# Kernel optimization log

Measured on AMD Instinct MI355X. Metric: run time of the kernel, lower is better.

Reference implementation:

```python
import jax, jax.numpy as jnp
import numpy as np

C, H, W = 16, 128, 128   # in_features, dim0, dim1
FD, OUT, POOL = 3, 64, 2  # filter_dim, out_features, pooling
B = 32


def setup_inputs() -> dict:
    key = jax.random.key(0)
    k1, k2, k3 = jax.random.split(key, 3)
    x = jax.random.normal(k1, (B, C, H, W), dtype=jnp.float32)
    # linear_layer: weight (in*fd^2, out) scaled by 1/sqrt(in*fd^2), bias (out,)
    weight = jax.random.normal(k2, (C * FD * FD, OUT), dtype=jnp.float32) / jnp.sqrt(
        jnp.float32(C * FD * FD))
    bias = jax.random.normal(k3, (OUT,), dtype=jnp.float32)
    return {"x": x, "weight": weight, "bias": bias}


def reference(x, weight, bias):
    # The one-hot isometry tensordot + reshape is exactly im2col with patch
    # vector ordering c*FD^2 + n*FD + m, so the whole convolution() equals a
    # VALID conv with kernel[o, c, n, m] = weight[c*FD^2 + n*FD + m, o].
    kernel = weight.reshape(C, FD, FD, OUT).transpose(3, 0, 1, 2)  # OIHW
    y = jax.lax.conv_general_dilated(
        x, kernel, window_strides=(1, 1), padding='VALID',
        dimension_numbers=('NCHW', 'OIHW', 'NCHW'))  # (B, OUT, n_conv, m_conv)
    y = jax.nn.relu(y + bias[None, :, None, None])
    b, o, hc, wc = y.shape  # hc = H-FD+1 = 126
    # block max-pool POOLxPOOL (crop to multiple of POOL, as in the original)
    hp, wp = hc // POOL, wc // POOL
    y = y[:, :, :hp * POOL, :wp * POOL].reshape(b, o, hp, POOL, wp, POOL)
    y = jnp.max(y, axis=(3, 5))  # (B, OUT, hp, wp)
    return y.reshape(b, o, -1)  # (B, OUT, hp*wp)
```

## Files before the change

kernel.cpp:

```cpp
#include <hip/hip_runtime.h>


typedef _Float16 f16x8 __attribute__((ext_vector_type(8)));
typedef float f32x16 __attribute__((ext_vector_type(16)));

#define MFMA16(A, B, C) __builtin_amdgcn_mfma_f32_32x32x16_f16(A, B, C, 0, 0, 0)

__global__ void convert_w(const float* __restrict__ weight, char* __restrict__ ws) {
  int tau = blockIdx.x * 256 + threadIdx.x;
  if (tau >= 1152) return;
  int t = tau >> 7, r = tau & 127, o = r >> 1, hf = r & 1;
  _Float16 h[8];
#pragma unroll
  for (int j = 0; j < 8; ++j)
    h[j] = (_Float16)weight[((hf * 8 + j) * 9 + t) * 64 + o];
  int off = (t * 2 + (o >> 5)) * 1024 + (hf * 32 + (o & 31)) * 16;
  *(f16x8*)(ws + off) = *(f16x8*)h;
}

__device__ __forceinline__ void compute_step(const char* lds, const f16x8 W[9][2],
                                             f32x16 acc[2][2], int i2, int xbase) {
#pragma unroll
  for (int q = 0; q < 16; ++q) {
    acc[0][0][q] = 0.f; acc[0][1][q] = 0.f;
    acc[1][0][q] = 0.f; acc[1][1][q] = 0.f;
  }
  __builtin_amdgcn_s_setprio(1);
#pragma unroll
  for (int t = 0; t < 9; ++t) {
    const int n = t / 3, m = t - 3 * n;
    const int a0 = (i2 + n) * 4096 + xbase + m * 16;
    const int a1 = a0 + 4096;
    f16x8 X0 = *(const f16x8*)(lds + a0);
    f16x8 X1 = *(const f16x8*)(lds + a1);
    acc[0][0] = MFMA16(W[t][0], X0, acc[0][0]);
    acc[1][0] = MFMA16(W[t][1], X0, acc[1][0]);
    acc[0][1] = MFMA16(W[t][0], X1, acc[0][1]);
    acc[1][1] = MFMA16(W[t][1], X1, acc[1][1]);
  }
  __builtin_amdgcn_s_setprio(0);
}

__device__ __forceinline__ void epilogue(const f32x16 acc[2][2],
                                         const float* __restrict__ bias,
                                         float* __restrict__ out, int b, int pr,
                                         int wv, int lane) {
  const int c31 = lane & 31;
  const int half = lane >> 5;
  const int pw = wv * 16 + (c31 >> 1);
  const bool doit = ((c31 & 1) == 0) && (pw < 63);
  const int obase = ((b * 64) * 63 + pr) * 63 + pw;
#pragma unroll
  for (int ot = 0; ot < 2; ++ot) {
#pragma unroll
    for (int q = 0; q < 16; ++q) {
      const int o0 = ot * 32 + (q & 3) + 8 * (q >> 2);
      float v = fmaxf(acc[ot][0][q], acc[ot][1][q]);
      v = fmaxf(v, __shfl_xor(v, 1, 64));
      float bv = half ? bias[o0 + 4] : bias[o0];
      v = fmaxf(v + bv, 0.0f);
      if (doit) out[obase + (o0 + 4 * half) * 3969] = v;
    }
  }
}

__global__ __launch_bounds__(256, 3)
void convpool_main(const float* __restrict__ x, const char* __restrict__ ws,
                   const float* __restrict__ bias, float* __restrict__ out) {
  __shared__ __align__(16) char lds[24640];
  const int tid = threadIdx.x;
  const int s = blockIdx.x;
  const int b = blockIdx.y;
  const int rb = 4 * s;
  const bool two = (s < 31);
  const int nr = two ? 6 : 4;
  const int lane = tid & 63;
  const int wv = tid >> 6;
  const int colS = tid >> 1;
  const int hfS = tid & 1;
  const float* xb = x + (b * 16 + hfS * 8) * 16384 + colS;

  float pv[6][8];
#pragma unroll
  for (int r = 0; r < 6; ++r)
    if (r < nr) {
#pragma unroll
      for (int j = 0; j < 8; ++j) pv[r][j] = xb[j * 16384 + (rb + r) * 128];
    }

  f16x8 W[9][2];
#pragma unroll
  for (int t = 0; t < 9; ++t)
#pragma unroll
    for (int ot = 0; ot < 2; ++ot)
      W[t][ot] = *(const f16x8*)(ws + (t * 2 + ot) * 1024 + lane * 16);

#pragma unroll
  for (int r = 0; r < 6; ++r)
    if (r < nr) {
      _Float16 h[8];
#pragma unroll
      for (int j = 0; j < 8; ++j) h[j] = (_Float16)pv[r][j];
      *(f16x8*)(lds + r * 4096 + hfS * 2048 + colS * 16) = *(f16x8*)h;
    }
  __syncthreads();

  const int xbase = (lane >> 5) * 2048 + (wv * 32 + (lane & 31)) * 16;
  f32x16 acc[2][2];

  compute_step(lds, W, acc, 0, xbase);
  epilogue(acc, bias, out, b, 2 * s, wv, lane);
  if (two) {
    compute_step(lds, W, acc, 2, xbase);
    epilogue(acc, bias, out, b, 2 * s + 1, wv, lane);
  }
}

extern "C" void kernel_launch(void* const* d_in, const int* in_sizes, int n_in,
                              void* d_out, int out_size, void* d_ws, size_t ws_size,
                              hipStream_t stream) {
  const float* x = (const float*)d_in[0];
  const float* wgt = (const float*)d_in[1];
  const float* bias = (const float*)d_in[2];
  float* out = (float*)d_out;
  char* ws = (char*)d_ws;
  convert_w<<<dim3(5), 256, 0, stream>>>(wgt, ws);
  convpool_main<<<dim3(32, 32), 256, 0, stream>>>(x, ws, bias, out);
}
```

Measured before the change: 45.13 us.

## Split work per block to one pooled row and one output-channel half

Each block now computes a single pooled output row for half of the output channels, so the grid grows from 32x32 to 126x32 blocks. Weights for that half are staged through LDS instead of being held in registers, which cuts register use and allows the launch bound to rise to 4 blocks per CU. In exchange, every block reloads its 4 input rows, so global reads of x rise roughly fourfold, and the input conversion is repeated across the channel halves.

```diff
diff --git a/kernel.cpp b/kernel.cpp
--- a/kernel.cpp
+++ b/kernel.cpp
@@ -18,101 +18,82 @@
   *(f16x8*)(ws + off) = *(f16x8*)h;
 }
 
-__device__ __forceinline__ void compute_step(const char* lds, const f16x8 W[9][2],
-                                             f32x16 acc[2][2], int i2, int xbase) {
+__global__ __launch_bounds__(256, 4)
+void convpool_main(const float* __restrict__ x, const char* __restrict__ ws,
+                   const float* __restrict__ bias, float* __restrict__ out) {
+  __shared__ __align__(16) char lds[25664];
+  const int tid = threadIdx.x;
+  const int bx = blockIdx.x;
+  const int pr = bx >> 1;
+  const int oh = bx & 1;
+  const int b = blockIdx.y;
+  const int lane = tid & 63;
+  const int wv = tid >> 6;
+  const int colS = tid >> 1;
+  const int hfS = tid & 1;
+  const float* xb = x + (b * 16 + hfS * 8) * 16384 + colS;
+
+  float pv[4][8];
 #pragma unroll
-  for (int q = 0; q < 16; ++q) {
-    acc[0][0][q] = 0.f; acc[0][1][q] = 0.f;
-    acc[1][0][q] = 0.f; acc[1][1][q] = 0.f;
+  for (int r = 0; r < 4; ++r)
+#pragma unroll
+    for (int j = 0; j < 8; ++j)
+      pv[r][j] = xb[j * 16384 + (2 * pr + r) * 128];
+
+  float4 wc[3];
+#pragma unroll
+  for (int k = 0; k < 3; ++k) {
+    int idx = tid + 256 * k;
+    if (idx < 576) {
+      int tap = idx >> 6, off = idx & 63;
+      wc[k] = *(const float4*)(ws + (tap * 2 + oh) * 1024 + off * 16);
+    }
   }
-  __builtin_amdgcn_s_setprio(1);
+
+#pragma unroll
+  for (int k = 0; k < 3; ++k) {
+    int idx = tid + 256 * k;
+    if (idx < 576) {
+      int tap = idx >> 6, off = idx & 63;
+      *(float4*)(lds + tap * 1024 + off * 16) = wc[k];
+    }
+  }
+#pragma unroll
+  for (int r = 0; r < 4; ++r) {
+    _Float16 h[8];
+#pragma unroll
+    for (int j = 0; j < 8; ++j) h[j] = (_Float16)pv[r][j];
+    *(f16x8*)(lds + 9216 + r * 4096 + hfS * 2048 + colS * 16) = *(f16x8*)h;
+  }
+  __syncthreads();
+
+  const int xbase = 9216 + (lane >> 5) * 2048 + (wv * 32 + (lane & 31)) * 16;
+  f32x16 a0, a1;
+#pragma unroll
+  for (int q = 0; q < 16; ++q) { a0[q] = 0.f; a1[q] = 0.f; }
 #pragma unroll
   for (int t = 0; t < 9; ++t) {
     const int n = t / 3, m = t - 3 * n;
-    const int a0 = (i2 + n) * 4096 + xbase + m * 16;
-    const int a1 = a0 + 4096;
-    f16x8 X0 = *(const f16x8*)(lds + a0);
-    f16x8 X1 = *(const f16x8*)(lds + a1);
-    acc[0][0] = MFMA16(W[t][0], X0, acc[0][0]);
-    acc[1][0] = MFMA16(W[t][1], X0, acc[1][0]);
-    acc[0][1] = MFMA16(W[t][0], X1, acc[0][1]);
-    acc[1][1] = MFMA16(W[t][1], X1, acc[1][1]);
+    f16x8 Wt = *(const f16x8*)(lds + t * 1024 + lane * 16);
+    f16x8 X0 = *(const f16x8*)(lds + n * 4096 + xbase + m * 16);
+    f16x8 X1 = *(const f16x8*)(lds + (n + 1) * 4096 + xbase + m * 16);
+    a0 = MFMA16(Wt, X0, a0);
+    a1 = MFMA16(Wt, X1, a1);
   }
-  __builtin_amdgcn_s_setprio(0);
-}
 
-__device__ __forceinline__ void epilogue(const f32x16 acc[2][2],
-                                         const float* __restrict__ bias,
-                                         float* __restrict__ out, int b, int pr,
-                                         int wv, int lane) {
   const int c31 = lane & 31;
   const int half = lane >> 5;
   const int pw = wv * 16 + (c31 >> 1);
   const bool doit = ((c31 & 1) == 0) && (pw < 63);
   const int obase = ((b * 64) * 63 + pr) * 63 + pw;
 #pragma unroll
-  for (int ot = 0; ot < 2; ++ot) {
-#pragma unroll
-    for (int q = 0; q < 16; ++q) {
-      const int o0 = ot * 32 + (q & 3) + 8 * (q >> 2);
-      float v = fmaxf(acc[ot][0][q], acc[ot][1][q]);
-      v = fmaxf(v, __shfl_xor(v, 1, 64));
-      float bv = half ? bias[o0 + 4] : bias[o0];
-      v = fmaxf(v + bv, 0.0f);
-      if (doit) out[obase + (o0 + 4 * half) * 3969] = v;
-    }
-  }
-}
-
-__global__ __launch_bounds__(256, 3)
-void convpool_main(const float* __restrict__ x, const char* __restrict__ ws,
-                   const float* __restrict__ bias, float* __restrict__ out) {
-  __shared__ __align__(16) char lds[24640];
-  const int tid = threadIdx.x;
-  const int s = blockIdx.x;
-  const int b = blockIdx.y;
-  const int rb = 4 * s;
-  const bool two = (s < 31);
-  const int nr = two ? 6 : 4;
-  const int lane = tid & 63;
-  const int wv = tid >> 6;
-  const int colS = tid >> 1;
-  const int hfS = tid & 1;
-  const float* xb = x + (b * 16 + hfS * 8) * 16384 + colS;
-
-  float pv[6][8];
-#pragma unroll
-  for (int r = 0; r < 6; ++r)
-    if (r < nr) {
-#pragma unroll
-      for (int j = 0; j < 8; ++j) pv[r][j] = xb[j * 16384 + (rb + r) * 128];
-    }
-
-  f16x8 W[9][2];
-#pragma unroll
-  for (int t = 0; t < 9; ++t)
-#pragma unroll
-    for (int ot = 0; ot < 2; ++ot)
-      W[t][ot] = *(const f16x8*)(ws + (t * 2 + ot) * 1024 + lane * 16);
-
-#pragma unroll
-  for (int r = 0; r < 6; ++r)
-    if (r < nr) {
-      _Float16 h[8];
-#pragma unroll
-      for (int j = 0; j < 8; ++j) h[j] = (_Float16)pv[r][j];
-      *(f16x8*)(lds + r * 4096 + hfS * 2048 + colS * 16) = *(f16x8*)h;
-    }
-  __syncthreads();
-
-  const int xbase = (lane >> 5) * 2048 + (wv * 32 + (lane & 31)) * 16;
-  f32x16 acc[2][2];
-
-  compute_step(lds, W, acc, 0, xbase);
-  epilogue(acc, bias, out, b, 2 * s, wv, lane);
-  if (two) {
-    compute_step(lds, W, acc, 2, xbase);
-    epilogue(acc, bias, out, b, 2 * s + 1, wv, lane);
+  for (int q = 0; q < 16; ++q) {
+    const int o0 = oh * 32 + (q & 3) + 8 * (q >> 2);
+    float v = fmaxf(a0[q], a1[q]);
+    v = fmaxf(v, __shfl_xor(v, 1, 64));
+    float bv = half ? bias[o0 + 4] : bias[o0];
+    v = fmaxf(v + bv, 0.0f);
+    if (doit) out[obase + (o0 + 4 * half) * 3969] = v;
   }
 }
 
@@ -125,5 +106,5 @@
   float* out = (float*)d_out;
   char* ws = (char*)d_ws;
   convert_w<<<dim3(5), 256, 0, stream>>>(wgt, ws);
-  convpool_main<<<dim3(32, 32), 256, 0, stream>>>(x, ws, bias, out);
+  convpool_main<<<dim3(126, 32), 256, 0, stream>>>(x, ws, bias, out);
 }
```

After: 53.65 us. 18.9% more time.

## Pre-convert input to fp16 workspace and stream tiles via direct global-to-LDS loads

Applied to the files above, without the earlier changes.

Adds a pre-pass kernel that converts the whole fp32 input to a channel-interleaved fp16 layout in workspace, alongside the weight conversion. The main kernel then loads rows straight into LDS with global_load_lds, so it no longer converts in registers. Each block now handles 8 input rows and 4 pooled rows in a loop instead of 2, which cuts halo re-reads. The cost is an extra full pass that reads the fp32 input and writes 16 MB of fp16, plus larger LDS use per block.

```diff
diff --git a/kernel.cpp b/kernel.cpp
--- a/kernel.cpp
+++ b/kernel.cpp
@@ -5,114 +5,106 @@
 typedef float f32x16 __attribute__((ext_vector_type(16)));
 
 #define MFMA16(A, B, C) __builtin_amdgcn_mfma_f32_32x32x16_f16(A, B, C, 0, 0, 0)
+#define XH_BYTES 16777216
 
-__global__ void convert_w(const float* __restrict__ weight, char* __restrict__ ws) {
-  int tau = blockIdx.x * 256 + threadIdx.x;
-  if (tau >= 1152) return;
-  int t = tau >> 7, r = tau & 127, o = r >> 1, hf = r & 1;
-  _Float16 h[8];
+#define GLOAD_LDS16(g, l)                                                    \
+  __builtin_amdgcn_global_load_lds(                                          \
+      (const __attribute__((address_space(1))) void*)(g),                    \
+      (__attribute__((address_space(3))) void*)(l), 16, 0, 0)
+
+__global__ void convert_xw(const float* __restrict__ x,
+                           const float* __restrict__ weight,
+                           char* __restrict__ ws) {
+  const int n = blockIdx.x;
+  if (n < 4096) {
+    const int g = n * 256 + threadIdx.x;
+    const int hf = g & 1, col = (g >> 1) & 127, row = (g >> 8) & 127, b = g >> 15;
+    _Float16 h[8];
 #pragma unroll
-  for (int j = 0; j < 8; ++j)
-    h[j] = (_Float16)weight[((hf * 8 + j) * 9 + t) * 64 + o];
-  int off = (t * 2 + (o >> 5)) * 1024 + (hf * 32 + (o & 31)) * 16;
-  *(f16x8*)(ws + off) = *(f16x8*)h;
-}
-
-__device__ __forceinline__ void compute_step(const char* lds, const f16x8 W[9][2],
-                                             f32x16 acc[2][2], int i2, int xbase) {
+    for (int j = 0; j < 8; ++j)
+      h[j] = (_Float16)x[((b * 16 + hf * 8 + j) * 128 + row) * 128 + col];
+    *(f16x8*)(ws + g * 16) = *(f16x8*)h;
+  } else {
+    const int tau = (n - 4096) * 256 + threadIdx.x;
+    if (tau >= 1152) return;
+    const int t = tau >> 7, r = tau & 127, o = r >> 1, hf = r & 1;
+    _Float16 h[8];
 #pragma unroll
-  for (int q = 0; q < 16; ++q) {
-    acc[0][0][q] = 0.f; acc[0][1][q] = 0.f;
-    acc[1][0][q] = 0.f; acc[1][1][q] = 0.f;
-  }
-  __builtin_amdgcn_s_setprio(1);
-#pragma unroll
-  for (int t = 0; t < 9; ++t) {
-    const int n = t / 3, m = t - 3 * n;
-    const int a0 = (i2 + n) * 4096 + xbase + m * 16;
-    const int a1 = a0 + 4096;
-    f16x8 X0 = *(const f16x8*)(lds + a0);
-    f16x8 X1 = *(const f16x8*)(lds + a1);
-    acc[0][0] = MFMA16(W[t][0], X0, acc[0][0]);
-    acc[1][0] = MFMA16(W[t][1], X0, acc[1][0]);
-    acc[0][1] = MFMA16(W[t][0], X1, acc[0][1]);
-    acc[1][1] = MFMA16(W[t][1], X1, acc[1][1]);
-  }
-  __builtin_amdgcn_s_setprio(0);
-}
-
-__device__ __forceinline__ void epilogue(const f32x16 acc[2][2],
-                                         const float* __restrict__ bias,
-                                         float* __restrict__ out, int b, int pr,
-                                         int wv, int lane) {
-  const int c31 = lane & 31;
-  const int half = lane >> 5;
-  const int pw = wv * 16 + (c31 >> 1);
-  const bool doit = ((c31 & 1) == 0) && (pw < 63);
-  const int obase = ((b * 64) * 63 + pr) * 63 + pw;
-#pragma unroll
-  for (int ot = 0; ot < 2; ++ot) {
-#pragma unroll
-    for (int q = 0; q < 16; ++q) {
-      const int o0 = ot * 32 + (q & 3) + 8 * (q >> 2);
-      float v = fmaxf(acc[ot][0][q], acc[ot][1][q]);
-      v = fmaxf(v, __shfl_xor(v, 1, 64));
-      float bv = half ? bias[o0 + 4] : bias[o0];
-      v = fmaxf(v + bv, 0.0f);
-      if (doit) out[obase + (o0 + 4 * half) * 3969] = v;
-    }
+    for (int j = 0; j < 8; ++j)
+      h[j] = (_Float16)weight[((hf * 8 + j) * 9 + t) * 64 + o];
+    const int off = (t * 2 + (o >> 5)) * 1024 + (hf * 32 + (o & 31)) * 16;
+    *(f16x8*)(ws + XH_BYTES + off) = *(f16x8*)h;
   }
 }
 
 __global__ __launch_bounds__(256, 3)
-void convpool_main(const float* __restrict__ x, const char* __restrict__ ws,
-                   const float* __restrict__ bias, float* __restrict__ out) {
-  __shared__ __align__(16) char lds[24640];
+void convpool_main(const char* __restrict__ ws, const float* __restrict__ bias,
+                   float* __restrict__ out) {
+  __shared__ __align__(16) char lds[41024];
   const int tid = threadIdx.x;
   const int s = blockIdx.x;
   const int b = blockIdx.y;
-  const int rb = 4 * s;
-  const bool two = (s < 31);
-  const int nr = two ? 6 : 4;
+  const int nsteps = (s < 15) ? 4 : 3;
+  const int rb = 8 * s;
   const int lane = tid & 63;
-  const int wv = tid >> 6;
-  const int colS = tid >> 1;
-  const int hfS = tid & 1;
-  const float* xb = x + (b * 16 + hfS * 8) * 16384 + colS;
+  const int ph = tid >> 6;
+  const int half = lane >> 5;
+  const int c31 = lane & 31;
 
-  float pv[6][8];
+  const char* xrow = ws + (size_t)(b * 128 + rb) * 4096 + tid * 16;
 #pragma unroll
-  for (int r = 0; r < 6; ++r)
-    if (r < nr) {
-#pragma unroll
-      for (int j = 0; j < 8; ++j) pv[r][j] = xb[j * 16384 + (rb + r) * 128];
-    }
+  for (int r = 0; r < 10; ++r)
+    if (rb + r < 128)
+      GLOAD_LDS16(xrow + r * 4096, lds + r * 4096 + tid * 16);
 
+  const char* wsW = ws + XH_BYTES;
   f16x8 W[9][2];
 #pragma unroll
   for (int t = 0; t < 9; ++t)
 #pragma unroll
     for (int ot = 0; ot < 2; ++ot)
-      W[t][ot] = *(const f16x8*)(ws + (t * 2 + ot) * 1024 + lane * 16);
+      W[t][ot] = *(const f16x8*)(wsW + (t * 2 + ot) * 1024 + lane * 16);
 
-#pragma unroll
-  for (int r = 0; r < 6; ++r)
-    if (r < nr) {
-      _Float16 h[8];
-#pragma unroll
-      for (int j = 0; j < 8; ++j) h[j] = (_Float16)pv[r][j];
-      *(f16x8*)(lds + r * 4096 + hfS * 2048 + colS * 16) = *(f16x8*)h;
-    }
   __syncthreads();
 
-  const int xbase = (lane >> 5) * 2048 + (wv * 32 + (lane & 31)) * 16;
-  f32x16 acc[2][2];
+  const int xoff = (ph * 32 + c31) * 32 + half * 16;
+  const int pw = ph * 16 + (c31 >> 1);
+  const bool doit = ((c31 & 1) == 0) && (pw < 63);
 
-  compute_step(lds, W, acc, 0, xbase);
-  epilogue(acc, bias, out, b, 2 * s, wv, lane);
-  if (two) {
-    compute_step(lds, W, acc, 2, xbase);
-    epilogue(acc, bias, out, b, 2 * s + 1, wv, lane);
+  for (int i = 0; i < nsteps; ++i) {
+    f32x16 acc[2][2];
+#pragma unroll
+    for (int q = 0; q < 16; ++q) {
+      acc[0][0][q] = 0.f; acc[0][1][q] = 0.f;
+      acc[1][0][q] = 0.f; acc[1][1][q] = 0.f;
+    }
+    __builtin_amdgcn_s_setprio(1);
+#pragma unroll
+    for (int t = 0; t < 9; ++t) {
+      const int n = t / 3, m = t - 3 * n;
+      const int a0 = (2 * i + n) * 4096 + xoff + m * 32;
+      f16x8 X0 = *(const f16x8*)(lds + a0);
+      f16x8 X1 = *(const f16x8*)(lds + a0 + 4096);
+      acc[0][0] = MFMA16(W[t][0], X0, acc[0][0]);
+      acc[1][0] = MFMA16(W[t][1], X0, acc[1][0]);
+      acc[0][1] = MFMA16(W[t][0], X1, acc[0][1]);
+      acc[1][1] = MFMA16(W[t][1], X1, acc[1][1]);
+    }
+    __builtin_amdgcn_s_setprio(0);
+
+    const int p = 4 * s + i;
+    const int obase = ((b * 64) * 63 + p) * 63 + pw;
+#pragma unroll
+    for (int ot = 0; ot < 2; ++ot)
+#pragma unroll
+      for (int q = 0; q < 16; ++q) {
+        const int o0 = ot * 32 + (q & 3) + 8 * (q >> 2);
+        float v = fmaxf(acc[ot][0][q], acc[ot][1][q]);
+        v = fmaxf(v, __shfl_xor(v, 1, 64));
+        const float bv = half ? bias[o0 + 4] : bias[o0];
+        v = fmaxf(v + bv, 0.0f);
+        if (doit) out[obase + (o0 + 4 * half) * 3969] = v;
+      }
   }
 }
 
@@ -124,6 +116,6 @@
   const float* bias = (const float*)d_in[2];
   float* out = (float*)d_out;
   char* ws = (char*)d_ws;
-  convert_w<<<dim3(5), 256, 0, stream>>>(wgt, ws);
-  convpool_main<<<dim3(32, 32), 256, 0, stream>>>(x, ws, bias, out);
+  convert_xw<<<dim3(4101), 256, 0, stream>>>(x, wgt, ws);
+  convpool_main<<<dim3(16, 32), 256, 0, stream>>>(ws, bias, out);
 }
```

Result: faster. 44.07 us (-2.3%).
